# Kernel optimization log

Hardware: AMD Instinct MI355X
Metric: run time of the kernel (lower is better)

The kernel has to match this reference:

```python
import jax, jax.numpy as jnp
import numpy as np


def setup_inputs() -> dict:
    key = jax.random.key(0)
    k = jax.random.split(key, 5)
    B, L, D = 8, 2048, 256  # D = 2*d_model, c_len == q_len == L (required by source's s1 broadcast)
    c = jax.random.normal(k[0], (B, L, D), dtype=jnp.float32)
    q = jax.random.normal(k[1], (B, L, D), dtype=jnp.float32)
    c_weight = jax.random.normal(k[2], (D, 1), dtype=jnp.float32) * 0.05
    q_weight = jax.random.normal(k[3], (D, 1), dtype=jnp.float32) * 0.05
    cq_weight = jax.random.normal(k[4], (1, 1, D), dtype=jnp.float32) * 0.05
    bias = jnp.zeros((1,), dtype=jnp.float32)
    return {"c": c, "q": q, "c_weight": c_weight, "q_weight": q_weight,
            "cq_weight": cq_weight, "bias": bias}


def reference(c, q, c_weight, q_weight, cq_weight, bias):
    # Dropout omitted (identity) for a deterministic reference.
    # s0: [B, c_len, 1] -> broadcasts over q_len
    s0 = jnp.matmul(c, c_weight)                       # [B, L, 1]
    # s1 (faithful to source, which uses c here): [B, 1, c_len]
    s1 = jnp.swapaxes(jnp.matmul(c, q_weight), 1, 2)   # [B, 1, L]
    # s2: elementwise-scaled batched GEMM: [B, c_len, q_len]
    s2 = jnp.matmul(c * cq_weight, jnp.swapaxes(q, 1, 2))
    s = s0 + s1 + s2 + bias                            # broadcast sum + scalar bias
    return s
```

## Files before the change

### kernel.cpp

```cpp
#include <hip/hip_runtime.h>
#include <hip/hip_bf16.h>

#define B_ 8
#define L_ 2048
#define D_ 256

typedef __bf16 bf16x8 __attribute__((ext_vector_type(8)));
typedef float f32x4 __attribute__((ext_vector_type(4)));

static __device__ __forceinline__ unsigned short f2bf(float f) {
    unsigned int u = __builtin_bit_cast(unsigned int, f);
    unsigned int lsb = (u >> 16) & 1u;
    u += 0x7fffu + lsb;
    return (unsigned short)(u >> 16);
}

static __device__ __forceinline__ void gload_lds16(const void* g, void* l) {
    __builtin_amdgcn_global_load_lds(
        (const __attribute__((address_space(1))) unsigned int*)g,
        (__attribute__((address_space(3))) unsigned int*)l, 16, 0, 0);
}

__global__ __launch_bounds__(256) void prep_kernel(
    const float* __restrict__ c, const float* __restrict__ q,
    const float* __restrict__ cw, const float* __restrict__ qw,
    const float* __restrict__ cqw, const float* __restrict__ bias,
    unsigned short* __restrict__ Abf, unsigned short* __restrict__ Qbf,
    float* __restrict__ s0, float* __restrict__ s1)
{
    const int wave = threadIdx.x >> 6;
    const int lane = threadIdx.x & 63;
    const int row  = blockIdx.x * 4 + wave;

    const float4 cv  = *(const float4*)(c   + (size_t)row * D_ + lane * 4);
    const float4 qv  = *(const float4*)(q   + (size_t)row * D_ + lane * 4);
    const float4 wc  = *(const float4*)(cw  + lane * 4);
    const float4 wq  = *(const float4*)(qw  + lane * 4);
    const float4 wcq = *(const float4*)(cqw + lane * 4);

    ushort4 av, qb;
    av.x = f2bf(cv.x * wcq.x); av.y = f2bf(cv.y * wcq.y);
    av.z = f2bf(cv.z * wcq.z); av.w = f2bf(cv.w * wcq.w);
    qb.x = f2bf(qv.x); qb.y = f2bf(qv.y);
    qb.z = f2bf(qv.z); qb.w = f2bf(qv.w);
    *(ushort4*)(Abf + (size_t)row * D_ + lane * 4) = av;
    *(ushort4*)(Qbf + (size_t)row * D_ + lane * 4) = qb;

    float p0 = cv.x * wc.x + cv.y * wc.y + cv.z * wc.z + cv.w * wc.w;
    float p1 = cv.x * wq.x + cv.y * wq.y + cv.z * wq.z + cv.w * wq.w;
    #pragma unroll
    for (int off = 32; off > 0; off >>= 1) {
        p0 += __shfl_down(p0, off);
        p1 += __shfl_down(p1, off);
    }
    if (lane == 0) { s0[row] = p0 + bias[0]; s1[row] = p1; }
}

#define BM 128
#define BN 128
#define BK 32
#define NSTEP (D_ / BK)

__global__ __launch_bounds__(256) void gemm_kernel(
    const unsigned short* __restrict__ A, const unsigned short* __restrict__ Q,
    const float* __restrict__ s0, const float* __restrict__ s1,
    float* __restrict__ out)
{
    __shared__ __align__(16) unsigned short As[3][BM * BK];
    __shared__ __align__(16) unsigned short Qs[3][BM * BK];

    const int tid  = threadIdx.x;
    const int wave = tid >> 6;
    const int lane = tid & 63;

    const int lin = blockIdx.x + (blockIdx.y << 4) + (blockIdx.z << 8);
    const int nl  = ((lin & 7) << 8) | (lin >> 3);
    const int b   = nl >> 8;
    const int brow = ((nl >> 4) & 15) * BM;
    const int bcol = (nl & 15) * BN;

    const unsigned short* Ab = A + ((size_t)b * L_ + brow) * D_;
    const unsigned short* Qb = Q + ((size_t)b * L_ + bcol) * D_;

    const int wr = wave >> 1;
    const int wc = wave & 1;

    const f32x4 zero = {0.f, 0.f, 0.f, 0.f};
    f32x4 acc[4][4];
    #pragma unroll
    for (int m = 0; m < 4; ++m)
        #pragma unroll
        for (int n = 0; n < 4; ++n) acc[m][n] = zero;

    auto stage = [&](int s) {
        const int k0 = s * BK;
        unsigned short* ab = &As[s % 3][0];
        unsigned short* qb = &Qs[s % 3][0];
        #pragma unroll
        for (int i = 0; i < 2; ++i) {
            const int sidx = i * 256 + wave * 64 + lane;
            const int row  = sidx >> 2;
            const int sl   = sidx & 3;
            const int ksrc = k0 + ((sl ^ ((row >> 1) & 3)) << 3);
            const int wbase = (i * 256 + wave * 64) * 8;
            gload_lds16(Ab + (size_t)row * D_ + ksrc, ab + wbase);
            gload_lds16(Qb + (size_t)row * D_ + ksrc, qb + wbase);
        }
    };

    auto compute = [&](int t) {
        const unsigned short* ab = &As[t % 3][0];
        const unsigned short* qb = &Qs[t % 3][0];
        bf16x8 af[4], qf[4];
        #pragma unroll
        for (int m = 0; m < 4; ++m) {
            const int row = wr * 64 + m * 16 + (lane & 15);
            const int idx = row * 32 + (((lane >> 4) ^ ((row >> 1) & 3)) << 3);
            af[m] = *(const bf16x8*)(ab + idx);
        }
        #pragma unroll
        for (int n = 0; n < 4; ++n) {
            const int row = wc * 64 + n * 16 + (lane & 15);
            const int idx = row * 32 + (((lane >> 4) ^ ((row >> 1) & 3)) << 3);
            qf[n] = *(const bf16x8*)(qb + idx);
        }
        __builtin_amdgcn_s_setprio(1);
        #pragma unroll
        for (int m = 0; m < 4; ++m)
            #pragma unroll
            for (int n = 0; n < 4; ++n)
                acc[m][n] = __builtin_amdgcn_mfma_f32_16x16x32_bf16(
                    af[m], qf[n], acc[m][n], 0, 0, 0);
        __builtin_amdgcn_s_setprio(0);
    };

    stage(0);
    stage(1);

    const int cohort = lin >> 8;
    if (cohort == 1 || cohort == 2) {
        const unsigned long long dl = (unsigned long long)cohort * 160ULL;
        const unsigned long long t0 = __builtin_amdgcn_s_memrealtime();
        while (__builtin_amdgcn_s_memrealtime() - t0 < dl)
            __builtin_amdgcn_s_sleep(2);
    }

#define STEP(T, VM) do {                                        \
        if ((T) + 2 < NSTEP) stage((T) + 2);                    \
        asm volatile("s_waitcnt vmcnt(" #VM ")" ::: "memory");  \
        __builtin_amdgcn_s_barrier();                           \
        asm volatile("" ::: "memory");                          \
        compute(T);                                             \
        asm volatile("" ::: "memory");                          \
        __builtin_amdgcn_s_barrier();                           \
        asm volatile("" ::: "memory");                          \
    } while (0)

    STEP(0, 8); STEP(1, 8); STEP(2, 8); STEP(3, 8);
    STEP(4, 8); STEP(5, 8); STEP(6, 4); STEP(7, 0);
#undef STEP

    const float* s0b = s0 + b * L_ + brow;
    const float* s1b = s1 + b * L_ + bcol;
    float s1v[4];
    #pragma unroll
    for (int n = 0; n < 4; ++n) s1v[n] = s1b[wc * 64 + n * 16 + (lane & 15)];
    float* outb = out + ((size_t)b * L_ + brow) * L_ + bcol;
    #pragma unroll
    for (int m = 0; m < 4; ++m) {
        #pragma unroll
        for (int r = 0; r < 4; ++r) {
            const int i = wr * 64 + m * 16 + (lane >> 4) * 4 + r;
            const float s0v = s0b[i];
            float* orow = outb + (size_t)i * L_;
            #pragma unroll
            for (int n = 0; n < 4; ++n)
                orow[wc * 64 + n * 16 + (lane & 15)] = acc[m][n][r] + s0v + s1v[n];
        }
    }
}

__global__ void naive_kernel(const float* __restrict__ c, const float* __restrict__ q,
                             const float* __restrict__ cw, const float* __restrict__ qw,
                             const float* __restrict__ cqw, const float* __restrict__ bias,
                             float* __restrict__ out)
{
    const size_t total = (size_t)B_ * L_ * L_;
    for (size_t idx = (size_t)blockIdx.x * blockDim.x + threadIdx.x; idx < total;
         idx += (size_t)gridDim.x * blockDim.x) {
        const int b = (int)(idx / ((size_t)L_ * L_));
        const int rem = (int)(idx % ((size_t)L_ * L_));
        const int i = rem / L_, j = rem % L_;
        const float* ci = c + ((size_t)b * L_ + i) * D_;
        const float* cj = c + ((size_t)b * L_ + j) * D_;
        const float* qj = q + ((size_t)b * L_ + j) * D_;
        float acc = bias[0];
        for (int d = 0; d < D_; ++d)
            acc += ci[d] * cw[d] + cj[d] * qw[d] + ci[d] * cqw[d] * qj[d];
        out[idx] = acc;
    }
}

extern "C" void kernel_launch(void* const* d_in, const int* in_sizes, int n_in,
                              void* d_out, int out_size, void* d_ws, size_t ws_size,
                              hipStream_t stream) {
    const float* c    = (const float*)d_in[0];
    const float* q    = (const float*)d_in[1];
    const float* cw   = (const float*)d_in[2];
    const float* qw   = (const float*)d_in[3];
    const float* cqw  = (const float*)d_in[4];
    const float* bias = (const float*)d_in[5];
    float* out = (float*)d_out;

    const size_t bytesA = (size_t)B_ * L_ * D_ * 2;
    const size_t need   = 2 * bytesA + 2 * (size_t)B_ * L_ * 4;

    if (ws_size >= need) {
        unsigned short* Abf = (unsigned short*)d_ws;
        unsigned short* Qbf = (unsigned short*)((char*)d_ws + bytesA);
        float* s0 = (float*)((char*)d_ws + 2 * bytesA);
        float* s1 = s0 + (size_t)B_ * L_;
        prep_kernel<<<B_ * L_ / 4, 256, 0, stream>>>(c, q, cw, qw, cqw, bias,
                                                     Abf, Qbf, s0, s1);
        dim3 grid(L_ / BN, L_ / BM, B_);
        gemm_kernel<<<grid, 256, 0, stream>>>(Abf, Qbf, s0, s1, out);
    } else {
        naive_kernel<<<2048, 256, 0, stream>>>(c, q, cw, qw, cqw, bias, out);
    }
}
```

Baseline: 44.74 us.

## Halve GEMM row tile to 64 and use a 1D grid for higher occupancy

Shrinks the block tile from 128x128 to 64x128, so each wave now owns a 64x32 output strip with 8 accumulators instead of 16. The launch becomes a flat 4096-block 1D grid with a revised swizzle, and launch_bounds requests 4 blocks per CU. The staging loads, waitcnt values and staggered-start cohorts are adjusted to match. The aim is more resident blocks and better latency hiding on this store-bound output, at the cost of less operand reuse per block and more total Q tile loads.

```diff
diff --git a/kernel.cpp b/kernel.cpp
--- a/kernel.cpp
+++ b/kernel.cpp
@@ -56,71 +56,71 @@
     if (lane == 0) { s0[row] = p0 + bias[0]; s1[row] = p1; }
 }
 
-#define BM 128
+#define BM 64
 #define BN 128
 #define BK 32
 #define NSTEP (D_ / BK)
 
-__global__ __launch_bounds__(256) void gemm_kernel(
+__global__ __launch_bounds__(256, 4) void gemm_kernel(
     const unsigned short* __restrict__ A, const unsigned short* __restrict__ Q,
     const float* __restrict__ s0, const float* __restrict__ s1,
     float* __restrict__ out)
 {
     __shared__ __align__(16) unsigned short As[3][BM * BK];
-    __shared__ __align__(16) unsigned short Qs[3][BM * BK];
+    __shared__ __align__(16) unsigned short Qs[3][BN * BK];
 
     const int tid  = threadIdx.x;
     const int wave = tid >> 6;
     const int lane = tid & 63;
 
-    const int lin = blockIdx.x + (blockIdx.y << 4) + (blockIdx.z << 8);
-    const int nl  = ((lin & 7) << 8) | (lin >> 3);
-    const int b   = nl >> 8;
-    const int brow = ((nl >> 4) & 15) * BM;
+    const int lin = blockIdx.x;
+    const int nl  = ((lin & 7) << 9) | (lin >> 3);
+    const int b    = nl >> 9;
+    const int brow = ((nl >> 4) & 31) * BM;
     const int bcol = (nl & 15) * BN;
 
     const unsigned short* Ab = A + ((size_t)b * L_ + brow) * D_;
     const unsigned short* Qb = Q + ((size_t)b * L_ + bcol) * D_;
 
-    const int wr = wave >> 1;
-    const int wc = wave & 1;
-
-    const f32x4 zero = {0.f, 0.f, 0.f, 0.f};
-    f32x4 acc[4][4];
+    f32x4 acc[4][2];
     #pragma unroll
     for (int m = 0; m < 4; ++m)
         #pragma unroll
-        for (int n = 0; n < 4; ++n) acc[m][n] = zero;
+        for (int n = 0; n < 2; ++n) acc[m][n] = {0.f, 0.f, 0.f, 0.f};
 
     auto stage = [&](int s) {
         const int k0 = s * BK;
         unsigned short* ab = &As[s % 3][0];
         unsigned short* qb = &Qs[s % 3][0];
+        {
+            const int row  = tid >> 2;
+            const int sl   = tid & 3;
+            const int ksrc = k0 + ((sl ^ ((row >> 1) & 3)) << 3);
+            gload_lds16(Ab + (size_t)row * D_ + ksrc, ab + wave * 512);
+        }
         #pragma unroll
         for (int i = 0; i < 2; ++i) {
-            const int sidx = i * 256 + wave * 64 + lane;
+            const int sidx = i * 256 + tid;
             const int row  = sidx >> 2;
             const int sl   = sidx & 3;
             const int ksrc = k0 + ((sl ^ ((row >> 1) & 3)) << 3);
-            const int wbase = (i * 256 + wave * 64) * 8;
-            gload_lds16(Ab + (size_t)row * D_ + ksrc, ab + wbase);
-            gload_lds16(Qb + (size_t)row * D_ + ksrc, qb + wbase);
+            gload_lds16(Qb + (size_t)row * D_ + ksrc, qb + (i * 256 + wave * 64) * 8);
         }
     };
 
     auto compute = [&](int t) {
         const unsigned short* ab = &As[t % 3][0];
         const unsigned short* qb = &Qs[t % 3][0];
-        bf16x8 af[4], qf[4];
+        bf16x8 af[4], qf[2];
         #pragma unroll
         for (int m = 0; m < 4; ++m) {
-            const int row = wr * 64 + m * 16 + (lane & 15);
+            const int row = m * 16 + (lane & 15);
             const int idx = row * 32 + (((lane >> 4) ^ ((row >> 1) & 3)) << 3);
             af[m] = *(const bf16x8*)(ab + idx);
         }
         #pragma unroll
-        for (int n = 0; n < 4; ++n) {
-            const int row = wc * 64 + n * 16 + (lane & 15);
+        for (int n = 0; n < 2; ++n) {
+            const int row = wave * 32 + n * 16 + (lane & 15);
             const int idx = row * 32 + (((lane >> 4) ^ ((row >> 1) & 3)) << 3);
             qf[n] = *(const bf16x8*)(qb + idx);
         }
@@ -128,7 +128,7 @@
         #pragma unroll
         for (int m = 0; m < 4; ++m)
             #pragma unroll
-            for (int n = 0; n < 4; ++n)
+            for (int n = 0; n < 2; ++n)
                 acc[m][n] = __builtin_amdgcn_mfma_f32_16x16x32_bf16(
                     af[m], qf[n], acc[m][n], 0, 0, 0);
         __builtin_amdgcn_s_setprio(0);
@@ -137,8 +137,8 @@
     stage(0);
     stage(1);
 
-    const int cohort = lin >> 8;
-    if (cohort == 1 || cohort == 2) {
+    const int cohort = lin >> 10;
+    if (cohort != 0) {
         const unsigned long long dl = (unsigned long long)cohort * 160ULL;
         const unsigned long long t0 = __builtin_amdgcn_s_memrealtime();
         while (__builtin_amdgcn_s_memrealtime() - t0 < dl)
@@ -156,26 +156,26 @@
         asm volatile("" ::: "memory");                          \
     } while (0)
 
-    STEP(0, 8); STEP(1, 8); STEP(2, 8); STEP(3, 8);
-    STEP(4, 8); STEP(5, 8); STEP(6, 4); STEP(7, 0);
+    STEP(0, 6); STEP(1, 6); STEP(2, 6); STEP(3, 6);
+    STEP(4, 6); STEP(5, 6); STEP(6, 3); STEP(7, 0);
 #undef STEP
 
     const float* s0b = s0 + b * L_ + brow;
-    const float* s1b = s1 + b * L_ + bcol;
-    float s1v[4];
-    #pragma unroll
-    for (int n = 0; n < 4; ++n) s1v[n] = s1b[wc * 64 + n * 16 + (lane & 15)];
-    float* outb = out + ((size_t)b * L_ + brow) * L_ + bcol;
+    const float* s1b = s1 + b * L_ + bcol + wave * 32;
+    float s1v[2];
+    #pragma unroll
+    for (int n = 0; n < 2; ++n) s1v[n] = s1b[n * 16 + (lane & 15)];
+    float* outb = out + ((size_t)b * L_ + brow) * L_ + bcol + wave * 32;
     #pragma unroll
     for (int m = 0; m < 4; ++m) {
         #pragma unroll
         for (int r = 0; r < 4; ++r) {
-            const int i = wr * 64 + m * 16 + (lane >> 4) * 4 + r;
+            const int i = m * 16 + (lane >> 4) * 4 + r;
             const float s0v = s0b[i];
             float* orow = outb + (size_t)i * L_;
             #pragma unroll
-            for (int n = 0; n < 4; ++n)
-                orow[wc * 64 + n * 16 + (lane & 15)] = acc[m][n][r] + s0v + s1v[n];
+            for (int n = 0; n < 2; ++n)
+                orow[n * 16 + (lane & 15)] = acc[m][n][r] + s0v + s1v[n];
         }
     }
 }
@@ -222,8 +222,7 @@
         float* s1 = s0 + (size_t)B_ * L_;
         prep_kernel<<<B_ * L_ / 4, 256, 0, stream>>>(c, q, cw, qw, cqw, bias,
                                                      Abf, Qbf, s0, s1);
-        dim3 grid(L_ / BN, L_ / BM, B_);
-        gemm_kernel<<<grid, 256, 0, stream>>>(Abf, Qbf, s0, s1, out);
+        gemm_kernel<<<dim3(4096), 256, 0, stream>>>(Abf, Qbf, s0, s1, out);
     } else {
         naive_kernel<<<2048, 256, 0, stream>>>(c, q, cw, qw, cqw, bias, out);
     }
```

Measured after the change: 53.83 us. +20.3%, slower.
